# Kernel tuning notes

Measured on AMD Instinct MI355X. Metric: run time of the kernel, lower is better.

The kernel has to match this reference:

```python
import jax, jax.numpy as jnp
import numpy as np

N_DETS = 8192
DEG = 64
E = N_DETS * DEG
NUM_BLOCKS = 8
SHORTCUT = 128   # shortcutDim
RED = 32         # reducedDim
INNER = 64       # blockInnerDim = 2*32
PW_RAW = 9
PW_HID = 256
PW_OUT = 32


def setup_inputs() -> dict:
    key = jax.random.key(0)
    ks = jax.random.split(key, 24)
    # valid boxes: x2 > x1, y2 > y1
    x1 = jax.random.uniform(ks[0], (N_DETS, 1), jnp.float32, 0.0, 1000.0)
    y1 = jax.random.uniform(ks[1], (N_DETS, 1), jnp.float32, 0.0, 1000.0)
    w = jax.random.uniform(ks[2], (N_DETS, 1), jnp.float32, 8.0, 128.0)
    h = jax.random.uniform(ks[3], (N_DETS, 1), jnp.float32, 8.0, 128.0)
    dtBoxes = jnp.concatenate([x1, y1, x1 + w, y1 + h], axis=1)
    detScores = jax.random.uniform(ks[4], (N_DETS, 1), jnp.float32)
    # every detection has DEG neighbors (first one is itself) -> no empty segments
    cIdxs = jnp.repeat(jnp.arange(N_DETS, dtype=jnp.int32), DEG)
    nIdxs = jax.random.randint(ks[5], (E,), 0, N_DETS, dtype=jnp.int32)
    nIdxs = nIdxs.at[::DEG].set(jnp.arange(N_DETS, dtype=jnp.int32))
    detFeatures = jnp.zeros((N_DETS, SHORTCUT), jnp.float32)

    def lin(k, fan_in, fan_out):
        b = 1.0 / np.sqrt(fan_in)
        return jax.random.uniform(k, (fan_in, fan_out), jnp.float32, -b, b)

    inp = dict(detScores=detScores, dtBoxes=dtBoxes, detFeatures=detFeatures,
               cIdxs=cIdxs, nIdxs=nIdxs)
    # pairwise feature generator MLP: 9 -> 256 -> 256 -> 32 (ReLU after each)
    inp['pw_W0'] = lin(ks[6], PW_RAW, PW_HID); inp['pw_b0'] = jnp.zeros((PW_HID,), jnp.float32)
    inp['pw_W1'] = lin(ks[7], PW_HID, PW_HID); inp['pw_b1'] = jnp.zeros((PW_HID,), jnp.float32)
    inp['pw_W2'] = lin(ks[8], PW_HID, PW_OUT); inp['pw_b2'] = jnp.zeros((PW_OUT,), jnp.float32)
    # per-block params, stacked over NUM_BLOCKS
    B = NUM_BLOCKS
    inp['blk_fc1_W'] = jnp.stack([lin(jax.random.fold_in(ks[9], i), SHORTCUT, RED) for i in range(B)])
    inp['blk_fc1_b'] = jnp.zeros((B, RED), jnp.float32)
    inp['blk_pw1_W'] = jnp.stack([lin(jax.random.fold_in(ks[10], i), 3 * RED, INNER) for i in range(B)])
    inp['blk_pw1_b'] = jnp.zeros((B, INNER), jnp.float32)
    inp['blk_pw2_W'] = jnp.stack([lin(jax.random.fold_in(ks[11], i), INNER, INNER) for i in range(B)])
    inp['blk_pw2_b'] = jnp.zeros((B, INNER), jnp.float32)
    inp['blk_post_W'] = jnp.stack([jnp.stack([lin(jax.random.fold_in(ks[12], 2 * i + j), INNER, INNER) for j in range(2)]) for i in range(B)])
    inp['blk_post_b'] = jnp.zeros((B, 2, INNER), jnp.float32)
    inp['blk_out_W'] = jnp.stack([lin(jax.random.fold_in(ks[13], i), INNER, SHORTCUT) for i in range(B)])
    inp['blk_out_b'] = jnp.zeros((B, SHORTCUT), jnp.float32)
    return inp


def _pairwise_raw(detScores, dtBoxes, cIdxs, nIdxs):
    # box data (getBoxData)
    x1, y1, x2, y2 = (dtBoxes[:, i:i + 1] for i in range(4))
    w, h = x2 - x1, y2 - y1
    area = w * h
    c, n = cIdxs, nIdxs
    # per-edge IoU (dt_dt_iou gathered at (c,n))
    ix = jnp.maximum(0.0, jnp.minimum(x2[c], x2[n]) - jnp.maximum(x1[c], x1[n]))
    iy = jnp.maximum(0.0, jnp.minimum(y2[c], y2[n]) - jnp.maximum(y1[c], y1[n]))
    inter = ix * iy
    iou = inter / (area[c] + area[n] - inter)
    c_w, c_h, n_w, n_h = w[c], h[c], w[n], h[n]
    c_scale = (c_w + c_h) / 2.0
    c_cx, c_cy = x1[c] + c_w / 2.0, y1[c] + c_h / 2.0
    n_cx, n_cy = x1[n] + n_w / 2.0, y1[n] + n_h / 2.0
    x_dist = n_cx - c_cx
    y_dist = n_cy - c_cy
    l2_dist = jnp.sqrt(x_dist ** 2 + y_dist ** 2) / c_scale
    x_dist = x_dist / c_scale
    y_dist = y_dist / c_scale
    log2 = jnp.log(jnp.float32(2.0))
    w_diff = jnp.log(n_w / c_w) / log2
    h_diff = jnp.log(n_h / c_h) / log2
    aspect_diff = (jnp.log(n_w / n_h) - jnp.log(c_w / c_h)) / log2
    return jnp.concatenate([detScores[c], detScores[n], iou, x_dist, y_dist,
                            l2_dist, w_diff, h_diff, aspect_diff], axis=1)  # [E,9]


def reference(detScores, dtBoxes, detFeatures, pw_W0, pw_b0, pw_W1, pw_b1,
              pw_W2, pw_b2, blk_fc1_W, blk_fc1_b, blk_pw1_W, blk_pw1_b,
              blk_pw2_W, blk_pw2_b, blk_post_W, blk_post_b, blk_out_W,
              blk_out_b, cIdxs, nIdxs):
    relu = jax.nn.relu
    numDets = detFeatures.shape[0]
    raw = _pairwise_raw(detScores, dtBoxes, cIdxs, nIdxs)
    pf = relu(raw @ pw_W0 + pw_b0)
    pf = relu(pf @ pw_W1 + pw_b1)
    pairFeatures = relu(pf @ pw_W2 + pw_b2)  # [E,32]

    f = detFeatures
    for i in range(blk_fc1_W.shape[0]):
        f1 = relu(f @ blk_fc1_W[i] + blk_fc1_b[i])                       # [N,32]
        comb = jnp.concatenate([pairFeatures, f1[cIdxs], f1[nIdxs]], 1)  # [E,96]
        comb = relu(comb @ blk_pw1_W[i] + blk_pw1_b[i])
        comb = relu(comb @ blk_pw2_W[i] + blk_pw2_b[i])                  # [E,64]
        pooled = jax.ops.segment_max(comb, cIdxs, num_segments=numDets)  # [N,64]
        pooled = relu(pooled @ blk_post_W[i, 0] + blk_post_b[i, 0])
        pooled = relu(pooled @ blk_post_W[i, 1] + blk_post_b[i, 1])
        f = relu(f + pooled @ blk_out_W[i] + blk_out_b[i])               # [N,128]
    return f
```

## Files before the change

kernel.cpp:

```cpp
#include <hip/hip_runtime.h>
#include <hip/hip_bf16.h>

typedef _Float16 half8 __attribute__((ext_vector_type(8)));
typedef __fp16 fp16x2 __attribute__((ext_vector_type(2)));
typedef float f32x4 __attribute__((ext_vector_type(4)));

#define N_DETS 8192

#define OFF_W0P   0
#define OFF_W1P   8192
#define OFF_W2P   73728
#define OFF_FC1P  81920
#define OFF_PW1P  114688
#define OFF_PW2P  163840
#define OFF_POSTP 196608
#define OFF_OUTP  262144
#define OFF_F1A   327680
#define OFF_F1B   589824
#define OFF_PFP   1114112
#define OFF_FBUF_BYTES 35782656


__device__ inline f32x4 mfma16(half8 a, half8 b, f32x4 c){
  return __builtin_amdgcn_mfma_f32_16x16x32_f16(a, b, c, 0, 0, 0);
}
__device__ inline half8 ldg8(const _Float16* p){ return *(const half8*)p; }

__device__ inline unsigned pkrtz(float a, float b){
  union { fp16x2 h; unsigned u; } x;
  x.h = __builtin_amdgcn_cvt_pkrtz(a, b);
  return x.u;
}
__device__ inline unsigned hmax2u(unsigned a, unsigned b){
  unsigned r;
  asm("v_pk_max_f16 %0, %1, %2" : "=v"(r) : "v"(a), "v"(b));
  return r;
}
__device__ inline unsigned hadd2u(unsigned a, unsigned b){
  unsigned r;
  asm("v_pk_add_f16 %0, %1, %2" : "=v"(r) : "v"(a), "v"(b));
  return r;
}

__device__ inline half8 cvtpack(f32x4 A, f32x4 B){
  union { unsigned w[4]; half8 h; } r;
  r.w[0] = pkrtz(A[0], A[1]); r.w[1] = pkrtz(A[2], A[3]);
  r.w[2] = pkrtz(B[0], B[1]); r.w[3] = pkrtz(B[2], B[3]);
  return r.h;
}
__device__ inline half8 cvtpackbr(f32x4 A, f32x4 B, const unsigned* pb){
  union { unsigned w[4]; half8 h; } r;
  r.w[0] = pkrtz(A[0], A[1]); r.w[1] = pkrtz(A[2], A[3]);
  r.w[2] = pkrtz(B[0], B[1]); r.w[3] = pkrtz(B[2], B[3]);
#pragma unroll
  for (int i = 0; i < 4; ++i) r.w[i] = hmax2u(hadd2u(r.w[i], pb[i]), 0u);
  return r.h;
}
__device__ inline half8 cvtpackr(f32x4 A, f32x4 B){
  union { unsigned w[4]; half8 h; } r;
  r.w[0] = pkrtz(A[0], A[1]); r.w[1] = pkrtz(A[2], A[3]);
  r.w[2] = pkrtz(B[0], B[1]); r.w[3] = pkrtz(B[2], B[3]);
#pragma unroll
  for (int i = 0; i < 4; ++i) r.w[i] = hmax2u(r.w[i], 0u);
  return r.h;
}

__device__ inline void packB(const float* W, int Ksrc, int Nn, _Float16* dst, int sig){
  int ns = (Ksrc + 31) >> 5;
  int t = sig / (ns * 64);
  int rem = sig - t * ns * 64;
  int s = rem >> 6;
  int l = rem & 63;
  int col = t * 16 + (l & 15);
  int g = l >> 4;
  half8 v;
#pragma unroll
  for (int j = 0; j < 8; ++j){
    int k = s*32 + ((j>>2)<<4) + g*4 + (j&3);
    v[j] = (_Float16)((k < Ksrc) ? W[k * Nn + col] : 0.f);
  }
  *(half8*)(dst + sig * 8) = v;
}

__device__ inline void packW0(const float* W, const float* bias, _Float16* dst, int sig){
  int t = sig >> 6, l = sig & 63;
  int col = t * 16 + (l & 15);
  int g = l >> 4;
  half8 v;
#pragma unroll
  for (int j = 0; j < 8; ++j){
    int k = ((j>>2)<<4) + g*4 + (j&3);
    float x = 0.f;
    if (k < 9) x = W[k * 256 + col];
    else if (k == 9) x = bias[col];
    v[j] = (_Float16)x;
  }
  *(half8*)(dst + sig * 8) = v;
}

__global__ __launch_bounds__(256) void kPrep(const float* pwW0, const float* pwb0,
    const float* pwW1, const float* pwW2,
    const float* fc1W, const float* pw1W, const float* pw2W, const float* postW, const float* outW,
    _Float16* wsh){
  int sig = blockIdx.x * 256 + threadIdx.x;
  if (sig < 1024){ packW0(pwW0, pwb0, wsh + OFF_W0P, sig); return; }
  sig -= 1024;
  if (sig < 8192){ packB(pwW1, 256, 256, wsh + OFF_W1P, sig); return; }
  sig -= 8192;
  if (sig < 1024){ packB(pwW2, 256, 32, wsh + OFF_W2P, sig); return; }
  sig -= 1024;
  int i = sig / 3840;
  int q = sig - i * 3840;
  if (q < 512){ packB(fc1W + i*4096, 128, 32, wsh + OFF_FC1P + i*4096, q); return; }
  q -= 512;
  if (q < 768){ packB(pw1W + i*6144, 96, 64, wsh + OFF_PW1P + i*6144, q); return; }
  q -= 768;
  if (q < 512){ packB(pw2W + i*4096, 64, 64, wsh + OFF_PW2P + i*4096, q); return; }
  q -= 512;
  if (q < 512){ packB(postW + i*8192, 64, 64, wsh + OFF_POSTP + i*8192, q); return; }
  q -= 512;
  if (q < 512){ packB(postW + i*8192 + 4096, 64, 64, wsh + OFF_POSTP + i*8192 + 4096, q); return; }
  q -= 512;
  packB(outW + i*8192, 64, 128, wsh + OFF_OUTP + i*8192, q);
}

__global__ __launch_bounds__(256, 2) void kP(const float* scores, const float* boxes,
    const int* cI, const int* nI, const float* b1, const float* b2,
    const _Float16* W0p, const _Float16* W1p, const _Float16* W2p, _Float16* pfp){
  __shared__ __align__(16) _Float16 sbuf[2][8192];
  __shared__ __align__(16) _Float16 rawp[8192];
  int tid = threadIdx.x;
  int lane = tid & 63, wave = tid >> 6;
  const f32x4 fz = {0.f, 0.f, 0.f, 0.f};

  half8 w0ld[4], s0ld[4];
#pragma unroll
  for (int it = 0; it < 4; ++it){
    w0ld[it] = ldg8(W0p + it*2048 + tid*8);
    s0ld[it] = ldg8(W1p + it*2048 + tid*8);
  }
  {
    half8 z = {0,0,0,0,0,0,0,0};
#pragma unroll
    for (int it = 0; it < 4; ++it) *(half8*)(rawp + it*2048 + tid*8) = z;
  }
  __syncthreads();
  {
    int e = blockIdx.x*256 + tid;
    int c = cI[e], n = nI[e];
    float cx1 = boxes[c*4+0], cy1 = boxes[c*4+1], cx2 = boxes[c*4+2], cy2 = boxes[c*4+3];
    float nx1 = boxes[n*4+0], ny1 = boxes[n*4+1], nx2 = boxes[n*4+2], ny2 = boxes[n*4+3];
    float cw = cx2-cx1, ch = cy2-cy1, nw = nx2-nx1, nh = ny2-ny1;
    float ca = cw*ch, na = nw*nh;
    float ix = fmaxf(fminf(cx2,nx2) - fmaxf(cx1,nx1), 0.f);
    float iy = fmaxf(fminf(cy2,ny2) - fmaxf(cy1,ny1), 0.f);
    float inter = ix*iy;
    float iou = inter / (ca + na - inter);
    float cs = (cw + ch) * 0.5f;
    float xd = (nx1 + nw*0.5f) - (cx1 + cw*0.5f);
    float yd = (ny1 + nh*0.5f) - (cy1 + ch*0.5f);
    float l2 = sqrtf(xd*xd + yd*yd) / cs;
    float wd = log2f(nw/cw), hd = log2f(nh/ch);
    float ad = log2f(nw/nh) - log2f(cw/ch);
    float rv[10] = {scores[c], scores[n], iou, xd/cs, yd/cs, l2, wd, hd, ad, 1.0f};
    int base = (tid >> 4) * 512;
    int r = tid & 15;
#pragma unroll
    for (int k = 0; k < 10; ++k)
      rawp[base + (((k>>2)&3)*16 + r)*8 + (k&3)] = (_Float16)rv[k];
  }
#pragma unroll
  for (int it = 0; it < 4; ++it){
    *(half8*)(&sbuf[0][0] + it*2048 + tid*8) = w0ld[it];
    *(half8*)(&sbuf[1][0] + it*2048 + tid*8) = s0ld[it];
  }
  __syncthreads();

  half8 h0f[4][8];
  {
    half8 braw[4];
#pragma unroll
    for (int et = 0; et < 4; ++et)
      braw[et] = *(const half8*)(rawp + ((wave*4+et)*64 + lane)*8);
#pragma unroll
    for (int mp = 0; mp < 8; ++mp){
      half8 A0 = *(const half8*)(&sbuf[0][0] + (2*mp)*512   + lane*8);
      half8 A1 = *(const half8*)(&sbuf[0][0] + (2*mp+1)*512 + lane*8);
#pragma unroll
      for (int et = 0; et < 4; ++et){
        f32x4 a = mfma16(A0, braw[et], fz);
        f32x4 b = mfma16(A1, braw[et], fz);
        h0f[et][mp] = cvtpackr(a, b);
      }
    }
  }
  __syncthreads();

  int q = lane >> 4;
  f32x4 apf[4][2];
#pragma unroll
  for (int et = 0; et < 4; ++et){ apf[et][0] = fz; apf[et][1] = fz; }
  for (int mp = 0; mp < 8; ++mp){
    const _Float16* cur = &sbuf[(mp+1)&1][0];
    half8 stg[4];
    if (mp < 7){
#pragma unroll
      for (int it = 0; it < 4; ++it)
        stg[it] = ldg8(W1p + (mp+1)*8192 + it*2048 + tid*8);
    }
    f32x4 acc[4][2];
#pragma unroll
    for (int et = 0; et < 4; ++et){ acc[et][0] = fz; acc[et][1] = fz; }
#pragma unroll
    for (int s = 0; s < 8; ++s){
      half8 A0 = *(const half8*)(cur + s*512       + lane*8);
      half8 A1 = *(const half8*)(cur + (8+s)*512   + lane*8);
#pragma unroll
      for (int et = 0; et < 4; ++et){
        acc[et][0] = mfma16(A0, h0f[et][s], acc[et][0]);
        acc[et][1] = mfma16(A1, h0f[et][s], acc[et][1]);
      }
    }
    unsigned pb[4];
    pb[0] = pkrtz(b1[mp*32 + q*4 + 0], b1[mp*32 + q*4 + 1]);
    pb[1] = pkrtz(b1[mp*32 + q*4 + 2], b1[mp*32 + q*4 + 3]);
    pb[2] = pkrtz(b1[mp*32 + 16 + q*4 + 0], b1[mp*32 + 16 + q*4 + 1]);
    pb[3] = pkrtz(b1[mp*32 + 16 + q*4 + 2], b1[mp*32 + 16 + q*4 + 3]);
    half8 w2a = ldg8(W2p + mp*512 + lane*8);
    half8 w2b = ldg8(W2p + (8+mp)*512 + lane*8);
#pragma unroll
    for (int et = 0; et < 4; ++et){
      half8 h1f = cvtpackbr(acc[et][0], acc[et][1], pb);
      apf[et][0] = mfma16(w2a, h1f, apf[et][0]);
      apf[et][1] = mfma16(w2b, h1f, apf[et][1]);
    }
    if (mp < 7){
      _Float16* nxt = &sbuf[mp&1][0];
#pragma unroll
      for (int it = 0; it < 4; ++it)
        *(half8*)(nxt + it*2048 + tid*8) = stg[it];
    }
    __syncthreads();
  }
  unsigned pc[4];
  pc[0] = pkrtz(b2[q*4 + 0], b2[q*4 + 1]);
  pc[1] = pkrtz(b2[q*4 + 2], b2[q*4 + 3]);
  pc[2] = pkrtz(b2[16 + q*4 + 0], b2[16 + q*4 + 1]);
  pc[3] = pkrtz(b2[16 + q*4 + 2], b2[16 + q*4 + 3]);
#pragma unroll
  for (int et = 0; et < 4; ++et){
    half8 pf = cvtpackbr(apf[et][0], apf[et][1], pc);
    *(half8*)(pfp + (blockIdx.x*16 + wave*4 + et)*512 + lane*8) = pf;
  }
}

__global__ __launch_bounds__(256) void kF1(const float* detF, const _Float16* fc1p,
    const float* fb, _Float16* f1G){
  int lane = threadIdx.x & 63, wave = threadIdx.x >> 6;
  int q = lane >> 4, e = lane & 15;
  int det = (blockIdx.x * 4 + wave) * 16 + e;
  const f32x4 fz = {0.f, 0.f, 0.f, 0.f};
  half8 ff[4];
#pragma unroll
  for (int s = 0; s < 4; ++s){
    const float* p = detF + det*128 + s*32 + q*4;
    f32x4 x0 = *(const f32x4*)(p);
    f32x4 x1 = *(const f32x4*)(p + 16);
    union { unsigned w[4]; half8 h; } u;
    u.w[0] = pkrtz(x0[0], x0[1]); u.w[1] = pkrtz(x0[2], x0[3]);
    u.w[2] = pkrtz(x1[0], x1[1]); u.w[3] = pkrtz(x1[2], x1[3]);
    ff[s] = u.h;
  }
#pragma unroll
  for (int m = 0; m < 2; ++m){
    f32x4 a = fz;
#pragma unroll
    for (int s = 0; s < 4; ++s)
      a = mfma16(ldg8(fc1p + (m*4+s)*512 + lane*8), ff[s], a);
    f32x4 bv = *(const f32x4*)(fb + m*16 + q*4);
    unsigned u0 = pkrtz(fmaxf(a[0]+bv[0],0.f), fmaxf(a[1]+bv[1],0.f));
    unsigned u1 = pkrtz(fmaxf(a[2]+bv[2],0.f), fmaxf(a[3]+bv[3],0.f));
    *(unsigned*)(f1G + det*32 + q*8 + m*4)     = u0;
    *(unsigned*)(f1G + det*32 + q*8 + m*4 + 2) = u1;
  }
}

__global__ __launch_bounds__(256) void kBlk(const _Float16* pfp, const _Float16* f1in,
    _Float16* f1out, const int* nI, const _Float16* pw1p, const _Float16* pw2p,
    const _Float16* post0p, const _Float16* post1p, const _Float16* outp, const _Float16* fc1pn,
    const float* bb1, const float* bb2, const float* pb0, const float* pb1, const float* ob,
    const float* fbn, const float* fin, float* fout, int doF1){
  __shared__ __align__(16) _Float16 poolS[1024];
  int tid = threadIdx.x, lane = tid & 63, wave = tid >> 6;
  int q = lane >> 4, e = lane & 15;
  int bid = blockIdx.x;
  int base = ((bid & 7) * 64 + (bid >> 3)) * 16;
  const f32x4 fz = {0.f, 0.f, 0.f, 0.f};

  half8 aW1[4][3], aW2[4][2];
  f32x4 b1v[4];
  unsigned b2p[8];
#pragma unroll
  for (int m = 0; m < 4; ++m){
#pragma unroll
    for (int k = 0; k < 3; ++k) aW1[m][k] = ldg8(pw1p + (m*3+k)*512 + lane*8);
#pragma unroll
    for (int k = 0; k < 2; ++k) aW2[m][k] = ldg8(pw2p + (m*2+k)*512 + lane*8);
    b1v[m] = *(const f32x4*)(bb1 + m*16 + q*4);
    b2p[m*2+0] = pkrtz(bb2[m*16 + q*4 + 0], bb2[m*16 + q*4 + 1]);
    b2p[m*2+1] = pkrtz(bb2[m*16 + q*4 + 2], bb2[m*16 + q*4 + 3]);
  }

  for (int dd = 0; dd < 4; ++dd){
    int d = wave*4 + dd;
    int det = base + d;
    half8 Bc = ldg8(f1in + det*32 + q*8);
    int nn[4];
#pragma unroll
    for (int et = 0; et < 4; ++et) nn[et] = nI[det*64 + et*16 + e];
    half8 Bpf[4], Bn[4];
#pragma unroll
    for (int et = 0; et < 4; ++et){
      Bpf[et] = ldg8(pfp + (det*4+et)*512 + lane*8);
      Bn[et]  = ldg8(f1in + nn[et]*32 + q*8);
    }
    f32x4 bcb[4];
#pragma unroll
    for (int m = 0; m < 4; ++m){
      f32x4 dc = mfma16(aW1[m][1], Bc, fz);
#pragma unroll
      for (int r = 0; r < 4; ++r) bcb[m][r] = dc[r] + b1v[m][r];
    }
    unsigned pm[8];
#pragma unroll
    for (int i = 0; i < 8; ++i) pm[i] = 0xFC00FC00u;
#pragma unroll
    for (int et = 0; et < 4; ++et){
      f32x4 acc[4];
#pragma unroll
      for (int m = 0; m < 4; ++m){
        acc[m] = mfma16(aW1[m][0], Bpf[et], fz);
        acc[m] = mfma16(aW1[m][2], Bn[et], acc[m]);
      }
      f32x4 r0, r1, r2, r3;
#pragma unroll
      for (int r = 0; r < 4; ++r){
        r0[r] = fmaxf(acc[0][r] + bcb[0][r], 0.f);
        r1[r] = fmaxf(acc[1][r] + bcb[1][r], 0.f);
        r2[r] = fmaxf(acc[2][r] + bcb[2][r], 0.f);
        r3[r] = fmaxf(acc[3][r] + bcb[3][r], 0.f);
      }
      half8 h1a = cvtpack(r0, r1);
      half8 h1b = cvtpack(r2, r3);
      f32x4 a2[4];
#pragma unroll
      for (int m = 0; m < 4; ++m){
        a2[m] = mfma16(aW2[m][0], h1a, fz);
        a2[m] = mfma16(aW2[m][1], h1b, a2[m]);
      }
      union { half8 h; unsigned w[4]; } uA, uB;
      uA.h = cvtpack(a2[0], a2[1]);
      uB.h = cvtpack(a2[2], a2[3]);
#pragma unroll
      for (int i = 0; i < 4; ++i){
        pm[i]   = hmax2u(pm[i],   uA.w[i]);
        pm[4+i] = hmax2u(pm[4+i], uB.w[i]);
      }
    }
#pragma unroll
    for (int s = 1; s <= 8; s <<= 1){
#pragma unroll
      for (int i = 0; i < 8; ++i)
        pm[i] = hmax2u(pm[i], __shfl_xor(pm[i], s));
    }
#pragma unroll
    for (int i = 0; i < 8; ++i)
      pm[i] = hmax2u(hadd2u(pm[i], b2p[i]), 0u);
    if (e == 0){
      union { unsigned w[4]; half8 h; } o0, o1;
#pragma unroll
      for (int i = 0; i < 4; ++i){ o0.w[i] = pm[i]; o1.w[i] = pm[4+i]; }
      *(half8*)(poolS + d*32 + q*8)       = o0.h;
      *(half8*)(poolS + 512 + d*32 + q*8) = o1.h;
    }
  }
  __syncthreads();

  half8 Bp0 = *(const half8*)(poolS + e*32 + q*8);
  half8 Bp1 = *(const half8*)(poolS + 512 + e*32 + q*8);
  int det = base + e;
  f32x4 t0[4];
#pragma unroll
  for (int m = 0; m < 4; ++m){
    f32x4 a = mfma16(ldg8(post0p + (m*2)*512   + lane*8), Bp0, fz);
    a = mfma16(ldg8(post0p + (m*2+1)*512 + lane*8), Bp1, a);
    f32x4 bv = *(const f32x4*)(pb0 + m*16 + q*4);
#pragma unroll
    for (int r = 0; r < 4; ++r) t0[m][r] = fmaxf(a[r] + bv[r], 0.f);
  }
  half8 p1a = cvtpack(t0[0], t0[1]);
  half8 p1b = cvtpack(t0[2], t0[3]);
#pragma unroll
  for (int m = 0; m < 4; ++m){
    f32x4 a = mfma16(ldg8(post1p + (m*2)*512   + lane*8), p1a, fz);
    a = mfma16(ldg8(post1p + (m*2+1)*512 + lane*8), p1b, a);
    f32x4 bv = *(const f32x4*)(pb1 + m*16 + q*4);
#pragma unroll
    for (int r = 0; r < 4; ++r) t0[m][r] = fmaxf(a[r] + bv[r], 0.f);
  }
  half8 p2a = cvtpack(t0[0], t0[1]);
  half8 p2b = cvtpack(t0[2], t0[3]);
  if (wave == 0){
    f32x4 fr[8];
#pragma unroll
    for (int m = 0; m < 8; ++m){
      f32x4 a = mfma16(ldg8(outp + (m*2)*512   + lane*8), p2a, fz);
      a = mfma16(ldg8(outp + (m*2+1)*512 + lane*8), p2b, a);
      f32x4 bv = *(const f32x4*)(ob + m*16 + q*4);
      f32x4 fv = *(const f32x4*)(fin + det*128 + m*16 + q*4);
#pragma unroll
      for (int r = 0; r < 4; ++r) fr[m][r] = fmaxf(fv[r] + a[r] + bv[r], 0.f);
    }
    *(f32x4*)(fout + det*128 + 0*16 + q*4) = fr[0];
    *(f32x4*)(fout + det*128 + 1*16 + q*4) = fr[1];
    if (doF1){
      half8 ff[4];
#pragma unroll
      for (int s = 0; s < 4; ++s) ff[s] = cvtpack(fr[2*s], fr[2*s+1]);
#pragma unroll
      for (int m = 0; m < 2; ++m){
        f32x4 a = fz;
#pragma unroll
        for (int s = 0; s < 4; ++s)
          a = mfma16(ldg8(fc1pn + (m*4+s)*512 + lane*8), ff[s], a);
        f32x4 bv = *(const f32x4*)(fbn + m*16 + q*4);
        unsigned u0 = pkrtz(fmaxf(a[0]+bv[0],0.f), fmaxf(a[1]+bv[1],0.f));
        unsigned u1 = pkrtz(fmaxf(a[2]+bv[2],0.f), fmaxf(a[3]+bv[3],0.f));
        *(unsigned*)(f1out + det*32 + q*8 + m*4)     = u0;
        *(unsigned*)(f1out + det*32 + q*8 + m*4 + 2) = u1;
      }
    }
  } else {
#pragma unroll
    for (int mm = 0; mm < 2; ++mm){
      int m = wave*2 + mm;
      f32x4 a = mfma16(ldg8(outp + (m*2)*512   + lane*8), p2a, fz);
      a = mfma16(ldg8(outp + (m*2+1)*512 + lane*8), p2b, a);
      f32x4 bv = *(const f32x4*)(ob + m*16 + q*4);
      f32x4 fv = *(const f32x4*)(fin + det*128 + m*16 + q*4);
      f32x4 fr;
#pragma unroll
      for (int r = 0; r < 4; ++r) fr[r] = fmaxf(fv[r] + a[r] + bv[r], 0.f);
      *(f32x4*)(fout + det*128 + m*16 + q*4) = fr;
    }
  }
}

extern "C" void kernel_launch(void* const* d_in, const int* in_sizes, int n_in,
                              void* d_out, int out_size, void* d_ws, size_t ws_size,
                              hipStream_t stream){
  const float* detScores   = (const float*)d_in[0];
  const float* dtBoxes     = (const float*)d_in[1];
  const float* detFeatures = (const float*)d_in[2];
  const int*   cI          = (const int*)d_in[3];
  const int*   nI          = (const int*)d_in[4];
  const float* pwW0 = (const float*)d_in[5];
  const float* pwb0 = (const float*)d_in[6];
  const float* pwW1 = (const float*)d_in[7];
  const float* pwb1 = (const float*)d_in[8];
  const float* pwW2 = (const float*)d_in[9];
  const float* pwb2 = (const float*)d_in[10];
  const float* fc1W = (const float*)d_in[11];
  const float* fc1b = (const float*)d_in[12];
  const float* pw1W = (const float*)d_in[13];
  const float* pw1b = (const float*)d_in[14];
  const float* pw2W = (const float*)d_in[15];
  const float* pw2b = (const float*)d_in[16];
  const float* postW = (const float*)d_in[17];
  const float* postb = (const float*)d_in[18];
  const float* outW  = (const float*)d_in[19];
  const float* outb  = (const float*)d_in[20];

  _Float16* wsh  = (_Float16*)d_ws;
  float*    fbuf = (float*)((char*)d_ws + OFF_FBUF_BYTES);
  _Float16* f1A  = wsh + OFF_F1A;
  _Float16* f1B  = wsh + OFF_F1B;
  _Float16* pfp  = wsh + OFF_PFP;

  kPrep<<<160, 256, 0, stream>>>(pwW0, pwb0, pwW1, pwW2, fc1W, pw1W, pw2W, postW, outW, wsh);
  kF1<<<128, 256, 0, stream>>>(detFeatures, wsh + OFF_FC1P, fc1b, f1A);
  kP<<<2048, 256, 0, stream>>>(detScores, dtBoxes, cI, nI, pwb1, pwb2,
      wsh + OFF_W0P, wsh + OFF_W1P, wsh + OFF_W2P, pfp);

  for (int i = 0; i < 8; ++i){
    int last = (i == 7);
    _Float16* fin1  = (i & 1) ? f1B : f1A;
    _Float16* fout1 = (i & 1) ? f1A : f1B;
    kBlk<<<512, 256, 0, stream>>>(pfp, fin1, fout1, nI,
        wsh + OFF_PW1P + i*6144, wsh + OFF_PW2P + i*4096,
        wsh + OFF_POSTP + i*8192, wsh + OFF_POSTP + i*8192 + 4096, wsh + OFF_OUTP + i*8192,
        wsh + OFF_FC1P + ((i+1) & 7)*4096,
        pw1b + i*64, pw2b + i*64, postb + i*128, postb + i*128 + 64, outb + i*128,
        fc1b + ((i+1) & 7)*32,
        (i == 0) ? detFeatures : fbuf, last ? (float*)d_out : fbuf, last ? 0 : 1);
  }
}
```

Measured before the change: 241.9 us.

## Prefetch next detection's indices and rebalance output MMA across waves via LDS

Software-prefetches the neighbor indices and center f1 row for the next detection while processing the current one, so the dependent gather latency is hidden, and disables unrolling of the detection loop. It also splits the 128-wide output projection evenly across the four waves (two 16-row tiles each) instead of wave 0 doing all eight. The fc1 input for the next block is then exchanged through shared memory with an extra barrier. This removes wave 0's serialized tail at the cost of more LDS traffic, a sync, and higher register pressure from the prefetch.

```diff
diff --git a/kernel.cpp b/kernel.cpp
--- a/kernel.cpp
+++ b/kernel.cpp
@@ -291,6 +291,7 @@
     const float* bb1, const float* bb2, const float* pb0, const float* pb1, const float* ob,
     const float* fbn, const float* fin, float* fout, int doF1){
   __shared__ __align__(16) _Float16 poolS[1024];
+  __shared__ __align__(16) _Float16 ffS[2048];
   int tid = threadIdx.x, lane = tid & 63, wave = tid >> 6;
   int q = lane >> 4, e = lane & 15;
   int bid = blockIdx.x;
@@ -311,23 +312,34 @@
     b2p[m*2+1] = pkrtz(bb2[m*16 + q*4 + 2], bb2[m*16 + q*4 + 3]);
   }
 
+  int nnC[4]; half8 BcC;
+  {
+    int det0 = base + wave*4;
+#pragma unroll
+    for (int et = 0; et < 4; ++et) nnC[et] = nI[det0*64 + et*16 + e];
+    BcC = ldg8(f1in + det0*32 + q*8);
+  }
+#pragma unroll 1
   for (int dd = 0; dd < 4; ++dd){
     int d = wave*4 + dd;
     int det = base + d;
-    half8 Bc = ldg8(f1in + det*32 + q*8);
-    int nn[4];
-#pragma unroll
-    for (int et = 0; et < 4; ++et) nn[et] = nI[det*64 + et*16 + e];
     half8 Bpf[4], Bn[4];
 #pragma unroll
     for (int et = 0; et < 4; ++et){
       Bpf[et] = ldg8(pfp + (det*4+et)*512 + lane*8);
-      Bn[et]  = ldg8(f1in + nn[et]*32 + q*8);
+      Bn[et]  = ldg8(f1in + nnC[et]*32 + q*8);
+    }
+    int nnN[4]; half8 BcN;
+    if (dd < 3){
+      int detn = det + 1;
+#pragma unroll
+      for (int et = 0; et < 4; ++et) nnN[et] = nI[detn*64 + et*16 + e];
+      BcN = ldg8(f1in + detn*32 + q*8);
     }
     f32x4 bcb[4];
 #pragma unroll
     for (int m = 0; m < 4; ++m){
-      f32x4 dc = mfma16(aW1[m][1], Bc, fz);
+      f32x4 dc = mfma16(aW1[m][1], BcC, fz);
 #pragma unroll
       for (int r = 0; r < 4; ++r) bcb[m][r] = dc[r] + b1v[m][r];
     }
@@ -383,6 +395,11 @@
       *(half8*)(poolS + d*32 + q*8)       = o0.h;
       *(half8*)(poolS + 512 + d*32 + q*8) = o1.h;
     }
+    if (dd < 3){
+#pragma unroll
+      for (int et = 0; et < 4; ++et) nnC[et] = nnN[et];
+      BcC = BcN;
+    }
   }
   __syncthreads();
 
@@ -410,48 +427,45 @@
   }
   half8 p2a = cvtpack(t0[0], t0[1]);
   half8 p2b = cvtpack(t0[2], t0[3]);
-  if (wave == 0){
-    f32x4 fr[8];
-#pragma unroll
-    for (int m = 0; m < 8; ++m){
-      f32x4 a = mfma16(ldg8(outp + (m*2)*512   + lane*8), p2a, fz);
-      a = mfma16(ldg8(outp + (m*2+1)*512 + lane*8), p2b, a);
-      f32x4 bv = *(const f32x4*)(ob + m*16 + q*4);
-      f32x4 fv = *(const f32x4*)(fin + det*128 + m*16 + q*4);
-#pragma unroll
-      for (int r = 0; r < 4; ++r) fr[m][r] = fmaxf(fv[r] + a[r] + bv[r], 0.f);
-    }
-    *(f32x4*)(fout + det*128 + 0*16 + q*4) = fr[0];
-    *(f32x4*)(fout + det*128 + 1*16 + q*4) = fr[1];
-    if (doF1){
-      half8 ff[4];
-#pragma unroll
-      for (int s = 0; s < 4; ++s) ff[s] = cvtpack(fr[2*s], fr[2*s+1]);
+  int m0 = wave*2, m1 = m0 + 1;
+  f32x4 fr0, fr1;
+  {
+    f32x4 a = mfma16(ldg8(outp + (m0*2)*512   + lane*8), p2a, fz);
+    a = mfma16(ldg8(outp + (m0*2+1)*512 + lane*8), p2b, a);
+    f32x4 bv = *(const f32x4*)(ob + m0*16 + q*4);
+    f32x4 fv = *(const f32x4*)(fin + det*128 + m0*16 + q*4);
+#pragma unroll
+    for (int r = 0; r < 4; ++r) fr0[r] = fmaxf(fv[r] + a[r] + bv[r], 0.f);
+  }
+  {
+    f32x4 a = mfma16(ldg8(outp + (m1*2)*512   + lane*8), p2a, fz);
+    a = mfma16(ldg8(outp + (m1*2+1)*512 + lane*8), p2b, a);
+    f32x4 bv = *(const f32x4*)(ob + m1*16 + q*4);
+    f32x4 fv = *(const f32x4*)(fin + det*128 + m1*16 + q*4);
+#pragma unroll
+    for (int r = 0; r < 4; ++r) fr1[r] = fmaxf(fv[r] + a[r] + bv[r], 0.f);
+  }
+  *(f32x4*)(fout + det*128 + m0*16 + q*4) = fr0;
+  *(f32x4*)(fout + det*128 + m1*16 + q*4) = fr1;
+  if (doF1){
+    half8 ffw = cvtpack(fr0, fr1);
+    *(half8*)(ffS + wave*512 + lane*8) = ffw;
+    __syncthreads();
+    if (wave == 0){
 #pragma unroll
       for (int m = 0; m < 2; ++m){
         f32x4 a = fz;
 #pragma unroll
-        for (int s = 0; s < 4; ++s)
-          a = mfma16(ldg8(fc1pn + (m*4+s)*512 + lane*8), ff[s], a);
+        for (int s = 0; s < 4; ++s){
+          half8 fs = *(const half8*)(ffS + s*512 + lane*8);
+          a = mfma16(ldg8(fc1pn + (m*4+s)*512 + lane*8), fs, a);
+        }
         f32x4 bv = *(const f32x4*)(fbn + m*16 + q*4);
         unsigned u0 = pkrtz(fmaxf(a[0]+bv[0],0.f), fmaxf(a[1]+bv[1],0.f));
         unsigned u1 = pkrtz(fmaxf(a[2]+bv[2],0.f), fmaxf(a[3]+bv[3],0.f));
         *(unsigned*)(f1out + det*32 + q*8 + m*4)     = u0;
         *(unsigned*)(f1out + det*32 + q*8 + m*4 + 2) = u1;
       }
-    }
-  } else {
-#pragma unroll
-    for (int mm = 0; mm < 2; ++mm){
-      int m = wave*2 + mm;
-      f32x4 a = mfma16(ldg8(outp + (m*2)*512   + lane*8), p2a, fz);
-      a = mfma16(ldg8(outp + (m*2+1)*512 + lane*8), p2b, a);
-      f32x4 bv = *(const f32x4*)(ob + m*16 + q*4);
-      f32x4 fv = *(const f32x4*)(fin + det*128 + m*16 + q*4);
-      f32x4 fr;
-#pragma unroll
-      for (int r = 0; r < 4; ++r) fr[r] = fmaxf(fv[r] + a[r] + bv[r], 0.f);
-      *(f32x4*)(fout + det*128 + m*16 + q*4) = fr;
     }
   }
 }
```

Measured after the change: 237.1 us. -2.0%, faster.
